# Kernel tuning notes

Measured on AMD Instinct MI355X. Metric: run time of the kernel, lower is better.

Reference implementation:

```python
import jax, jax.numpy as jnp
import numpy as np

HIDDEN = 1024
HEADS = 16
HEAD_DIM = HIDDEN // HEADS
BATCH = 2
SEQ = 2048
ROPE_BASE = 10000.0


def rotate_half(x):
    x1, x2 = x[..., : x.shape[-1] // 2], x[..., x.shape[-1] // 2 :]
    return jnp.concatenate((-x2, x1), axis=-1)


def rope_cos_sin(seq_len, dim, dtype=jnp.float32):
    inv_freq = 1.0 / (ROPE_BASE ** (jnp.arange(0, dim, 2, dtype=jnp.float32) / dim))
    t = jnp.arange(seq_len, dtype=jnp.float32)
    freqs = jnp.einsum('i,j->ij', t, inv_freq)          # [S, dim/2]
    emb = jnp.concatenate((freqs, freqs), axis=-1)       # [S, dim]
    return emb.astype(dtype).cos(), emb.astype(dtype).sin() if False else (jnp.cos(emb).astype(dtype), jnp.sin(emb).astype(dtype))[0], None


def _rope(seq_len, dim):
    inv_freq = 1.0 / (ROPE_BASE ** (jnp.arange(0, dim, 2, dtype=jnp.float32) / dim))
    t = jnp.arange(seq_len, dtype=jnp.float32)
    freqs = jnp.einsum('i,j->ij', t, inv_freq)
    emb = jnp.concatenate((freqs, freqs), axis=-1)
    return jnp.cos(emb), jnp.sin(emb)  # each [S, dim]


def setup_inputs() -> dict:
    key = jax.random.key(0)
    ks = jax.random.split(key, 9)
    scale = 1.0 / np.sqrt(HIDDEN)
    inp = {
        'hidden_states': jax.random.normal(ks[0], (BATCH, SEQ, HIDDEN), dtype=jnp.float32),
        'Wq': jax.random.uniform(ks[1], (HIDDEN, HIDDEN), minval=-scale, maxval=scale, dtype=jnp.float32),
        'bq': jax.random.uniform(ks[2], (HIDDEN,), minval=-scale, maxval=scale, dtype=jnp.float32),
        'Wk': jax.random.uniform(ks[3], (HIDDEN, HIDDEN), minval=-scale, maxval=scale, dtype=jnp.float32),
        'bk': jax.random.uniform(ks[4], (HIDDEN,), minval=-scale, maxval=scale, dtype=jnp.float32),
        'Wv': jax.random.uniform(ks[5], (HIDDEN, HIDDEN), minval=-scale, maxval=scale, dtype=jnp.float32),
        'bv': jax.random.uniform(ks[6], (HIDDEN,), minval=-scale, maxval=scale, dtype=jnp.float32),
        'Wo': jax.random.uniform(ks[7], (HIDDEN, HIDDEN), minval=-scale, maxval=scale, dtype=jnp.float32),
        'bo': jax.random.uniform(ks[8], (HIDDEN,), minval=-scale, maxval=scale, dtype=jnp.float32),
    }
    return inp


def reference(hidden_states, Wq, bq, Wk, bk, Wv, bv, Wo, bo):
    B, S, H = hidden_states.shape
    # projections (torch Linear: x @ W.T + b), split into heads: [B, nH, S, hd]
    def proj(W, b):
        y = hidden_states @ W.T + b
        return y.reshape(B, S, HEADS, HEAD_DIM).transpose(0, 2, 1, 3)

    q = proj(Wq, bq)
    k = proj(Wk, bk)
    v = proj(Wv, bv)

    cos, sin = _rope(S, HEAD_DIM)  # [S, hd], broadcast over B, nH
    q = q * cos + rotate_half(q) * sin
    k = k * cos + rotate_half(k) * sin

    scale = 1.0 / jnp.sqrt(jnp.array(HEAD_DIM, dtype=q.dtype))
    logits = jnp.einsum('bhqd,bhkd->bhqk', q, k) * scale  # [B, nH, S, S]
    attn = jax.nn.softmax(logits, axis=-1)
    out = jnp.einsum('bhqk,bhkd->bhqd', attn, v)           # [B, nH, S, hd]
    out = out.transpose(0, 2, 1, 3).reshape(B, S, H)
    return out @ Wo.T + bo
```

## Files before the change

kernel.cpp:

```cpp
#include <hip/hip_runtime.h>
#include <hip/hip_bf16.h>
#include <math.h>

#define HIDDEN 1024
#define NH 16
#define HD 64
#define BATCH 2
#define SEQ 2048

typedef __attribute__((ext_vector_type(8))) short bf16x8;
typedef __attribute__((ext_vector_type(4))) float f32x4;

static __device__ __forceinline__ unsigned short f2b(float f) {
    __hip_bfloat16 h = __float2bfloat16(f);
    return __builtin_bit_cast(unsigned short, h);
}

static __device__ __forceinline__ float fexp2(float x) {
    return __builtin_amdgcn_exp2f(x);
}

static __device__ __forceinline__ void async16(const unsigned short* g, unsigned short* l) {
    __builtin_amdgcn_global_load_lds(
        (const __attribute__((address_space(1))) unsigned int*)g,
        (__attribute__((address_space(3))) unsigned int*)l, 16, 0, 0);
}

__global__ __launch_bounds__(256)
void cvt_bf16(const float* __restrict__ X,
              const float* __restrict__ Wq, const float* __restrict__ Wk,
              const float* __restrict__ Wv, const float* __restrict__ Wo,
              unsigned short* __restrict__ dst)
{
    const size_t g = (size_t)blockIdx.x * 256 + threadIdx.x;
    const float* src;
    size_t local;
    if (g < 1048576) {
        src = X; local = g;
    } else {
        const size_t gg = g - 1048576;
        const int r = (int)(gg >> 18);
        local = gg & 262143;
        src = (r == 0) ? Wq : ((r == 1) ? Wk : ((r == 2) ? Wv : Wo));
    }
    const float4 v = *(const float4*)(src + local * 4);
    ushort4 o;
    o.x = f2b(v.x); o.y = f2b(v.y); o.z = f2b(v.z); o.w = f2b(v.w);
    *(ushort4*)(dst + g * 4) = o;
}

__global__ __launch_bounds__(256, 2)
void qkv_rope(const unsigned short* __restrict__ X,
              const unsigned short* __restrict__ Wqb, const float* __restrict__ bq,
              const unsigned short* __restrict__ Wkb, const float* __restrict__ bk,
              const unsigned short* __restrict__ Wvb, const float* __restrict__ bv,
              unsigned short* __restrict__ qw, unsigned short* __restrict__ kw,
              unsigned short* __restrict__ vw)
{
    const int proj = blockIdx.y >> 3;
    const unsigned short* W = (proj == 0) ? Wqb : ((proj == 1) ? Wkb : Wvb);
    const float* bias       = (proj == 0) ? bq : ((proj == 1) ? bk : bv);
    unsigned short* outp    = (proj == 0) ? qw : ((proj == 1) ? kw : vw);
    const int tn = (blockIdx.y & 7) * 128;
    const int tm = blockIdx.x * 128;

    __shared__ __align__(16) unsigned short As[128 * 32];
    __shared__ __align__(16) unsigned short Bs[128 * 32];

    const int tid  = threadIdx.x;
    const int lane = tid & 63;
    const int wave = tid >> 6;
    const int quad = lane >> 4;
    const int l16  = lane & 15;
    const int wm   = (wave & 1) * 64;
    const int wn   = (wave >> 1) * 64;

    const int r0 = tid >> 2;
    const int c0 = (tid & 3) * 8;
    const unsigned short* Ag = X + (size_t)(tm + r0) * HIDDEN + c0;
    const unsigned short* Bg = W + (size_t)(tn + r0) * HIDDEN + c0;
    unsigned short* lA = As + tid * 8;
    unsigned short* lB = Bs + tid * 8;

    f32x4 acc[4][4] = {};

    for (int k0 = 0; k0 < HIDDEN; k0 += 32) {
        __syncthreads();
        async16(Ag + k0, lA);
        async16(Ag + 64 * HIDDEN + k0, lA + 2048);
        async16(Bg + k0, lB);
        async16(Bg + 64 * HIDDEN + k0, lB + 2048);
        __syncthreads();
        bf16x8 af[4], bfr[4];
#pragma unroll
        for (int i = 0; i < 4; ++i)
            af[i] = *(const bf16x8*)(As + (wm + i * 16 + l16) * 32 + quad * 8);
#pragma unroll
        for (int j = 0; j < 4; ++j)
            bfr[j] = *(const bf16x8*)(Bs + (wn + j * 16 + l16) * 32 + quad * 8);
#pragma unroll
        for (int i = 0; i < 4; ++i)
#pragma unroll
            for (int j = 0; j < 4; ++j)
                acc[i][j] = __builtin_amdgcn_mfma_f32_16x16x32_bf16(af[i], bfr[j], acc[i][j], 0, 0, 0);
    }

    const bool dorope = (proj < 2);
    float bsv[4];
#pragma unroll
    for (int j = 0; j < 4; ++j) bsv[j] = bias[tn + wn + j * 16 + l16];
    float inv_e = 0.f, inv_o = 0.f;
    if (dorope) {
        const float LB = 0.4152410118609203f;
        inv_e = exp2f(-LB * (float)l16);
        inv_o = exp2f(-LB * (float)(16 + l16));
    }
#pragma unroll
    for (int i = 0; i < 4; ++i) {
#pragma unroll
        for (int r = 0; r < 4; ++r) {
            const int m = tm + wm + i * 16 + quad * 4 + r;
            const int b = m >> 11;
            const int s = m & (SEQ - 1);
            float cs0 = 1.f, sn0 = 0.f, cs1 = 1.f, sn1 = 0.f;
            if (dorope) {
                const float sf = (float)s;
                __sincosf(sf * inv_e, &sn0, &cs0);
                __sincosf(sf * inv_o, &sn1, &cs1);
            }
#pragma unroll
            for (int j = 0; j < 4; ++j) {
                const int n = tn + wn + j * 16 + l16;
                const float v = acc[i][j][r] + bsv[j];
                float o = v;
                if (dorope) {
                    const float vp = acc[i][j ^ 2][r] + bsv[j ^ 2];
                    o = v * ((j & 1) ? cs1 : cs0) + ((j < 2) ? -vp : vp) * ((j & 1) ? sn1 : sn0);
                }
                const int h = n >> 6;
                const int d = n & 63;
                outp[(((size_t)(b * NH + h)) * SEQ + s) * HD + d] = f2b(o);
            }
        }
    }
}

__global__ __launch_bounds__(256, 2)
void attn_fwd(const unsigned short* __restrict__ qb, const unsigned short* __restrict__ kb,
              const unsigned short* __restrict__ vb, unsigned short* __restrict__ ob)
{
    const int flat  = blockIdx.y * gridDim.x + blockIdx.x;
    const int flat2 = (flat & 7) * 64 + (flat >> 3);
    const int bh = flat2 >> 4;
    const int qt = flat2 & 15;
    const int b  = bh >> 4;
    const int h  = bh & 15;
    const unsigned short* Q = qb + (size_t)bh * SEQ * HD;
    const unsigned short* K = kb + (size_t)bh * SEQ * HD;
    const unsigned short* V = vb + (size_t)bh * SEQ * HD;

    const int tid  = threadIdx.x;
    const int wave = tid >> 6;
    const int lane = tid & 63;
    const int quad = lane >> 4;
    const int l16  = lane & 15;
    const int q0   = qt * 128 + wave * 32;

    __shared__ __align__(16) unsigned short Pb[4][32 * 136];
    __shared__ __align__(16) unsigned short Vt[64 * 136];

    bf16x8 qf[2][2];
#pragma unroll
    for (int mt = 0; mt < 2; ++mt)
#pragma unroll
        for (int kk = 0; kk < 2; ++kk)
            qf[mt][kk] = *(const bf16x8*)(Q + (size_t)(q0 + mt * 16 + l16) * HD + kk * 32 + quad * 8);

    f32x4 oacc[2][4] = {};
    float mr[2][4], lr[2][4];
#pragma unroll
    for (int mt = 0; mt < 2; ++mt)
#pragma unroll
        for (int r = 0; r < 4; ++r) { mr[mt][r] = -3.0e38f; lr[mt][r] = 0.f; }

    const int vkey = tid >> 3;
    const int vd0  = (tid & 7) * 8;
    const int vm   = tid & 7;

    const float KSCL = 0.18033688011112042f;

    for (int kt = 0; kt < SEQ / 128; ++kt) {
        const int t0 = kt * 128;

        f32x4 sc[2][8] = {};
#pragma unroll
        for (int kk = 0; kk < 2; ++kk) {
            bf16x8 kf[8];
#pragma unroll
            for (int jj = 0; jj < 8; ++jj)
                kf[jj] = *(const bf16x8*)(K + (size_t)(t0 + jj * 16 + l16) * HD + kk * 32 + quad * 8);
#pragma unroll
            for (int mt = 0; mt < 2; ++mt)
#pragma unroll
                for (int jj = 0; jj < 8; ++jj)
                    sc[mt][jj] = __builtin_amdgcn_mfma_f32_16x16x32_bf16(qf[mt][kk], kf[jj], sc[mt][jj], 0, 0, 0);
        }

        __syncthreads();

#pragma unroll
        for (int p = 0; p < 4; ++p) {
            const int ky = vkey + 32 * p;
            const int cs = ky ^ (vm << 3);
            bf16x8 vv = *(const bf16x8*)(V + (size_t)(t0 + ky) * HD + vd0);
#pragma unroll
            for (int u = 0; u < 8; ++u)
                Vt[(vd0 + u) * 136 + cs] = ((const unsigned short*)&vv)[u];
        }

#pragma unroll
        for (int mt = 0; mt < 2; ++mt) {
#pragma unroll
            for (int r = 0; r < 4; ++r) {
                float mx = sc[mt][0][r];
#pragma unroll
                for (int jj = 1; jj < 8; ++jj) mx = fmaxf(mx, sc[mt][jj][r]);
                float ms = mx * KSCL;
#pragma unroll
                for (int off = 8; off; off >>= 1) ms = fmaxf(ms, __shfl_xor(ms, off));
                const float mold = mr[mt][r];
                const bool stable = __all(ms <= mold + 8.0f) != 0;
                const float mnew = stable ? mold : fmaxf(mold, ms);
                float ps = 0.f;
                const int prow = (mt * 16 + quad * 4 + r) * 136;
#pragma unroll
                for (int jj = 0; jj < 8; ++jj) {
                    const float p = fexp2(sc[mt][jj][r] * KSCL - mnew);
                    ps += p;
                    Pb[wave][prow + jj * 16 + l16] = f2b(p);
                }
#pragma unroll
                for (int off = 8; off; off >>= 1) ps += __shfl_xor(ps, off);
                if (stable) {
                    lr[mt][r] += ps;
                } else {
                    const float alpha = fexp2(mold - mnew);
                    mr[mt][r] = mnew;
                    lr[mt][r] = lr[mt][r] * alpha + ps;
#pragma unroll
                    for (int nn = 0; nn < 4; ++nn) oacc[mt][nn][r] *= alpha;
                }
            }
        }

        __syncthreads();

#pragma unroll
        for (int kk2 = 0; kk2 < 4; ++kk2) {
            bf16x8 pf[2], vf[4];
#pragma unroll
            for (int mt = 0; mt < 2; ++mt)
                pf[mt] = *(const bf16x8*)(&Pb[wave][(mt * 16 + l16) * 136 + kk2 * 32 + quad * 8]);
#pragma unroll
            for (int nn = 0; nn < 4; ++nn) {
                const int d   = nn * 16 + l16;
                const int mrd = (nn * 2 + (l16 >> 3)) & 7;
                const int cb  = (kk2 * 32 + quad * 8) ^ (mrd << 3);
                vf[nn] = *(const bf16x8*)(&Vt[d * 136 + cb]);
            }
#pragma unroll
            for (int mt = 0; mt < 2; ++mt)
#pragma unroll
                for (int nn = 0; nn < 4; ++nn)
                    oacc[mt][nn] = __builtin_amdgcn_mfma_f32_16x16x32_bf16(pf[mt], vf[nn], oacc[mt][nn], 0, 0, 0);
        }
    }

#pragma unroll
    for (int mt = 0; mt < 2; ++mt) {
#pragma unroll
        for (int r = 0; r < 4; ++r) {
            const float inv = 1.0f / lr[mt][r];
            const int s = q0 + mt * 16 + quad * 4 + r;
#pragma unroll
            for (int nn = 0; nn < 4; ++nn) {
                const int d = nn * 16 + l16;
                ob[((size_t)(b * SEQ + s)) * HIDDEN + h * HD + d] = f2b(oacc[mt][nn][r] * inv);
            }
        }
    }
}

__global__ __launch_bounds__(256, 2)
void out_proj(const unsigned short* __restrict__ A,
              const unsigned short* __restrict__ W,
              const float* __restrict__ bias,
              float* __restrict__ out)
{
    const int tn = blockIdx.y * 128;
    const int tm = blockIdx.x * 128;

    __shared__ __align__(16) unsigned short As[128 * 32];
    __shared__ __align__(16) unsigned short Bs[128 * 32];

    const int tid  = threadIdx.x;
    const int lane = tid & 63;
    const int wave = tid >> 6;
    const int quad = lane >> 4;
    const int l16  = lane & 15;
    const int wm   = (wave & 1) * 64;
    const int wn   = (wave >> 1) * 64;

    const int r0 = tid >> 2;
    const int c0 = (tid & 3) * 8;
    const unsigned short* Ag = A + (size_t)(tm + r0) * HIDDEN + c0;
    const unsigned short* Bg = W + (size_t)(tn + r0) * HIDDEN + c0;
    unsigned short* lA = As + tid * 8;
    unsigned short* lB = Bs + tid * 8;

    f32x4 acc[4][4] = {};

    for (int k0 = 0; k0 < HIDDEN; k0 += 32) {
        __syncthreads();
        async16(Ag + k0, lA);
        async16(Ag + 64 * HIDDEN + k0, lA + 2048);
        async16(Bg + k0, lB);
        async16(Bg + 64 * HIDDEN + k0, lB + 2048);
        __syncthreads();
        bf16x8 af[4], bfr[4];
#pragma unroll
        for (int i = 0; i < 4; ++i)
            af[i] = *(const bf16x8*)(As + (wm + i * 16 + l16) * 32 + quad * 8);
#pragma unroll
        for (int j = 0; j < 4; ++j)
            bfr[j] = *(const bf16x8*)(Bs + (wn + j * 16 + l16) * 32 + quad * 8);
#pragma unroll
        for (int i = 0; i < 4; ++i)
#pragma unroll
            for (int j = 0; j < 4; ++j)
                acc[i][j] = __builtin_amdgcn_mfma_f32_16x16x32_bf16(af[i], bfr[j], acc[i][j], 0, 0, 0);
    }

    float bsv[4];
#pragma unroll
    for (int j = 0; j < 4; ++j) bsv[j] = bias[tn + wn + j * 16 + l16];
#pragma unroll
    for (int i = 0; i < 4; ++i) {
#pragma unroll
        for (int r = 0; r < 4; ++r) {
            const int m = tm + wm + i * 16 + quad * 4 + r;
#pragma unroll
            for (int j = 0; j < 4; ++j) {
                const int n = tn + wn + j * 16 + l16;
                out[(size_t)m * HIDDEN + n] = acc[i][j][r] + bsv[j];
            }
        }
    }
}

extern "C" void kernel_launch(void* const* d_in, const int* in_sizes, int n_in,
                              void* d_out, int out_size, void* d_ws, size_t ws_size,
                              hipStream_t stream) {
    const float* hs = (const float*)d_in[0];
    const float* Wq = (const float*)d_in[1];
    const float* bq = (const float*)d_in[2];
    const float* Wk = (const float*)d_in[3];
    const float* bk = (const float*)d_in[4];
    const float* Wv = (const float*)d_in[5];
    const float* bv = (const float*)d_in[6];
    const float* Wo = (const float*)d_in[7];
    const float* bo = (const float*)d_in[8];
    float* out = (float*)d_out;

    unsigned short* Xb  = (unsigned short*)d_ws;
    unsigned short* Wqb = Xb + 4194304;
    unsigned short* Wkb = Wqb + 1048576;
    unsigned short* Wvb = Wkb + 1048576;
    unsigned short* Wob = Wvb + 1048576;
    unsigned short* qw  = Wob + 1048576;
    unsigned short* kw  = qw + 4194304;
    unsigned short* vw  = kw + 4194304;
    unsigned short* aw  = vw + 4194304;

    cvt_bf16<<<dim3(8192), 256, 0, stream>>>(hs, Wq, Wk, Wv, Wo, Xb);
    qkv_rope<<<dim3(32, 24), 256, 0, stream>>>(Xb, Wqb, bq, Wkb, bk, Wvb, bv, qw, kw, vw);
    attn_fwd<<<dim3(16, 32), 256, 0, stream>>>(qw, kw, vw, aw);
    out_proj<<<dim3(32, 8), 256, 0, stream>>>(aw, Wob, bo, out);
}
```

Measured before the change: 255.7 us.

## Halve attention block size and defer softmax row-sum reduction to epilogue

The attention kernel now uses 128-thread blocks covering 64 query rows each, so twice as many blocks are launched. The block-to-tile swizzle and V-tile staging loop are adjusted to match. The online-softmax path checks whether the max is stable once per tile with a single wave vote, rescales only when needed, and accumulates per-lane partial row sums. The cross-lane shuffle reduction of the sum moves to the final normalisation. Smaller blocks reload K/V tiles more often per query but should raise occupancy and cut per-tile shuffle work.

```diff
diff --git a/kernel.cpp b/kernel.cpp
--- a/kernel.cpp
+++ b/kernel.cpp
@@ -145,14 +145,14 @@
     }
 }
 
-__global__ __launch_bounds__(256, 2)
+__global__ __launch_bounds__(128, 4)
 void attn_fwd(const unsigned short* __restrict__ qb, const unsigned short* __restrict__ kb,
               const unsigned short* __restrict__ vb, unsigned short* __restrict__ ob)
 {
     const int flat  = blockIdx.y * gridDim.x + blockIdx.x;
-    const int flat2 = (flat & 7) * 64 + (flat >> 3);
-    const int bh = flat2 >> 4;
-    const int qt = flat2 & 15;
+    const int flat2 = (flat & 7) * 128 + (flat >> 3);
+    const int bh = flat2 >> 5;
+    const int qt = flat2 & 31;
     const int b  = bh >> 4;
     const int h  = bh & 15;
     const unsigned short* Q = qb + (size_t)bh * SEQ * HD;
@@ -164,9 +164,9 @@
     const int lane = tid & 63;
     const int quad = lane >> 4;
     const int l16  = lane & 15;
-    const int q0   = qt * 128 + wave * 32;
-
-    __shared__ __align__(16) unsigned short Pb[4][32 * 136];
+    const int q0   = qt * 64 + wave * 32;
+
+    __shared__ __align__(16) unsigned short Pb[2][32 * 136];
     __shared__ __align__(16) unsigned short Vt[64 * 136];
 
     bf16x8 qf[2][2];
@@ -209,8 +209,8 @@
         __syncthreads();
 
 #pragma unroll
-        for (int p = 0; p < 4; ++p) {
-            const int ky = vkey + 32 * p;
+        for (int p = 0; p < 8; ++p) {
+            const int ky = vkey + 16 * p;
             const int cs = ky ^ (vm << 3);
             bf16x8 vv = *(const bf16x8*)(V + (size_t)(t0 + ky) * HD + vd0);
 #pragma unroll
@@ -218,6 +218,7 @@
                 Vt[(vd0 + u) * 136 + cs] = ((const unsigned short*)&vv)[u];
         }
 
+        float dmax = -3.0e38f;
 #pragma unroll
         for (int mt = 0; mt < 2; ++mt) {
 #pragma unroll
@@ -225,31 +226,43 @@
                 float mx = sc[mt][0][r];
 #pragma unroll
                 for (int jj = 1; jj < 8; ++jj) mx = fmaxf(mx, sc[mt][jj][r]);
-                float ms = mx * KSCL;
-#pragma unroll
-                for (int off = 8; off; off >>= 1) ms = fmaxf(ms, __shfl_xor(ms, off));
-                const float mold = mr[mt][r];
-                const bool stable = __all(ms <= mold + 8.0f) != 0;
-                const float mnew = stable ? mold : fmaxf(mold, ms);
+                dmax = fmaxf(dmax, mx * KSCL - mr[mt][r]);
+            }
+        }
+        if (!__all(dmax <= 8.0f)) {
+#pragma unroll
+            for (int mt = 0; mt < 2; ++mt) {
+#pragma unroll
+                for (int r = 0; r < 4; ++r) {
+                    float mx = sc[mt][0][r];
+#pragma unroll
+                    for (int jj = 1; jj < 8; ++jj) mx = fmaxf(mx, sc[mt][jj][r]);
+                    float ms = mx * KSCL;
+#pragma unroll
+                    for (int off = 8; off; off >>= 1) ms = fmaxf(ms, __shfl_xor(ms, off));
+                    const float mnew  = fmaxf(mr[mt][r], ms);
+                    const float alpha = fexp2(mr[mt][r] - mnew);
+                    mr[mt][r] = mnew;
+                    lr[mt][r] *= alpha;
+#pragma unroll
+                    for (int nn = 0; nn < 4; ++nn) oacc[mt][nn][r] *= alpha;
+                }
+            }
+        }
+#pragma unroll
+        for (int mt = 0; mt < 2; ++mt) {
+#pragma unroll
+            for (int r = 0; r < 4; ++r) {
+                const float mnew = mr[mt][r];
                 float ps = 0.f;
                 const int prow = (mt * 16 + quad * 4 + r) * 136;
 #pragma unroll
                 for (int jj = 0; jj < 8; ++jj) {
-                    const float p = fexp2(sc[mt][jj][r] * KSCL - mnew);
+                    const float p = fexp2(fmaf(sc[mt][jj][r], KSCL, -mnew));
                     ps += p;
                     Pb[wave][prow + jj * 16 + l16] = f2b(p);
                 }
-#pragma unroll
-                for (int off = 8; off; off >>= 1) ps += __shfl_xor(ps, off);
-                if (stable) {
-                    lr[mt][r] += ps;
-                } else {
-                    const float alpha = fexp2(mold - mnew);
-                    mr[mt][r] = mnew;
-                    lr[mt][r] = lr[mt][r] * alpha + ps;
-#pragma unroll
-                    for (int nn = 0; nn < 4; ++nn) oacc[mt][nn][r] *= alpha;
-                }
+                lr[mt][r] += ps;
             }
         }
 
@@ -280,7 +293,10 @@
     for (int mt = 0; mt < 2; ++mt) {
 #pragma unroll
         for (int r = 0; r < 4; ++r) {
-            const float inv = 1.0f / lr[mt][r];
+            float ls = lr[mt][r];
+#pragma unroll
+            for (int off = 8; off; off >>= 1) ls += __shfl_xor(ls, off);
+            const float inv = 1.0f / ls;
             const int s = q0 + mt * 16 + quad * 4 + r;
 #pragma unroll
             for (int nn = 0; nn < 4; ++nn) {
@@ -384,6 +400,6 @@
 
     cvt_bf16<<<dim3(8192), 256, 0, stream>>>(hs, Wq, Wk, Wv, Wo, Xb);
     qkv_rope<<<dim3(32, 24), 256, 0, stream>>>(Xb, Wqb, bq, Wkb, bk, Wvb, bv, qw, kw, vw);
-    attn_fwd<<<dim3(16, 32), 256, 0, stream>>>(qw, kw, vw, aw);
+    attn_fwd<<<dim3(32, 32), 128, 0, stream>>>(qw, kw, vw, aw);
     out_proj<<<dim3(32, 8), 256, 0, stream>>>(aw, Wob, bo, out);
 }
```

Result: slower. 274.4 us (+7.3%).
